# Optimization experiments

Measured on AMD Instinct MI355X. Metric: run time of the kernel, lower is better.

Reference implementation:

```python
import jax, jax.numpy as jnp
import numpy as np

ORDER = 3
OS_FACTOR = 1.5
B, T, I, H = 32, 1024, 512, 512

def _lagrange_kernel(order, os_factor):
    # mirrors LagrangeInterp_RNN.__init__
    if os_factor >= 2:
        delta = os_factor - np.floor(os_factor) + 1
    else:
        delta = os_factor - 1
    k = np.ones(order + 1, dtype=np.float64)
    for n in range(order + 1):
        for j in range(order + 1):
            if j != n:
                k[n] *= (delta - j) / (n - j)
    return jnp.asarray(k, dtype=jnp.float32)

def setup_inputs() -> dict:
    key = jax.random.key(0)
    k1, k2, k3, k4, k5 = jax.random.split(key, 5)
    s = 1.0 / np.sqrt(H)
    return {
        "x": jax.random.normal(k1, (B, T, I), dtype=jnp.float32),
        "Wih": jax.random.uniform(k2, (H, I), minval=-s, maxval=s, dtype=jnp.float32),
        "Whh": jax.random.uniform(k3, (H, H), minval=-s, maxval=s, dtype=jnp.float32),
        "bih": jax.random.uniform(k4, (H,), minval=-s, maxval=s, dtype=jnp.float32),
        "bhh": jax.random.uniform(k5, (H,), minval=-s, maxval=s, dtype=jnp.float32),
        "kernel": _lagrange_kernel(ORDER, OS_FACTOR),
    }

def reference(x, Wih, Whh, bih, bhh, kernel):
    # x: [B, T, I]; kernel: [order+1]; prev_states: [B, order+1, H]
    b = x.shape[0]
    h_dim = Whh.shape[0]
    prev0 = jnp.zeros((b, kernel.shape[0], h_dim), dtype=x.dtype)
    # input projection is independent of the recurrence -> one big GEMM
    xproj = jnp.einsum('bti,hi->bth', x, Wih) + bih  # [B, T, H]

    def step(prev, xp_t):
        # Lagrange-interpolated read of the history window
        h_read = jnp.einsum('k,bkh->bh', kernel, prev)
        h = jnp.tanh(xp_t + h_read @ Whh.T + bhh)
        # torch code detaches the state stored into prev_states, then rolls
        # so the newest (detached) state sits at index 0 (epsilon == 1)
        new_prev = jnp.concatenate(
            [jax.lax.stop_gradient(h)[:, None, :], prev[:, :-1, :]], axis=1)
        return new_prev, h

    _, states_t = jax.lax.scan(step, prev0, jnp.swapaxes(xproj, 0, 1))
    states = jnp.swapaxes(states_t, 0, 1)  # [B, T, H]
    return states, states[:, -1, :]
```

## Files before the change

kernel.cpp:

```cpp
#include <hip/hip_runtime.h>

typedef __bf16 bf16x8 __attribute__((ext_vector_type(8)));
typedef float  f32x4  __attribute__((ext_vector_type(4)));
typedef unsigned long long u64;

#define AGENT __HIP_MEMORY_SCOPE_AGENT

__device__ __forceinline__ float fast_tanh(float x) {
    float e = __expf(2.0f * x);
    return 1.0f - 2.0f * __builtin_amdgcn_rcpf(e + 1.0f);
}

__global__ __launch_bounds__(256) void xproj_gemm_kernel(
    const float* __restrict__ x, const float* __restrict__ Wih,
    const float* __restrict__ bih, float* __restrict__ out)
{
    __shared__ __bf16 Ash[64][72];
    __shared__ __bf16 Bsh[64][72];

    const int tid  = threadIdx.x;
    const int wave = tid >> 6, lane = tid & 63;
    const int col  = lane & 15, kq = lane >> 4;
    const int bt0  = blockIdx.x * 64;
    const int h0   = blockIdx.y * 64;

    f32x4 acc[4];
#pragma unroll
    for (int nt = 0; nt < 4; ++nt) acc[nt] = (f32x4){0.f, 0.f, 0.f, 0.f};

    const int r  = tid >> 2;
    const int cb = (tid & 3) * 16;

    for (int k0 = 0; k0 < 512; k0 += 64) {
        const float* ax = x   + (size_t)(bt0 + r) * 512 + k0 + cb;
        const float* bx = Wih + (size_t)(h0  + r) * 512 + k0 + cb;
#pragma unroll
        for (int j = 0; j < 4; ++j) {
            const float4 av = ((const float4*)ax)[j];
            const float4 bv = ((const float4*)bx)[j];
            const int c = cb + 4 * j;
            Ash[r][c+0]=(__bf16)av.x; Ash[r][c+1]=(__bf16)av.y;
            Ash[r][c+2]=(__bf16)av.z; Ash[r][c+3]=(__bf16)av.w;
            Bsh[r][c+0]=(__bf16)bv.x; Bsh[r][c+1]=(__bf16)bv.y;
            Bsh[r][c+2]=(__bf16)bv.z; Bsh[r][c+3]=(__bf16)bv.w;
        }
        __syncthreads();
#pragma unroll
        for (int kt = 0; kt < 2; ++kt) {
            bf16x8 a = *(const bf16x8*)&Ash[wave * 16 + col][kt * 32 + kq * 8];
#pragma unroll
            for (int nt = 0; nt < 4; ++nt) {
                bf16x8 bb = *(const bf16x8*)&Bsh[nt * 16 + col][kt * 32 + kq * 8];
                acc[nt] = __builtin_amdgcn_mfma_f32_16x16x32_bf16(a, bb, acc[nt], 0, 0, 0);
            }
        }
        __syncthreads();
    }
#pragma unroll
    for (int nt = 0; nt < 4; ++nt) {
        const float bv = bih[h0 + nt * 16 + col];
#pragma unroll
        for (int reg = 0; reg < 4; ++reg) {
            const int m = bt0 + wave * 16 + kq * 4 + reg;
            out[(size_t)m * 512 + h0 + nt * 16 + col] = acc[nt][reg] + bv;
        }
    }
}

__global__ __launch_bounds__(256) void lagrange_rnn_kernel(
    const float* __restrict__ Whh, const float* __restrict__ bhh,
    const float* __restrict__ kern, float* __restrict__ out,
    u64* __restrict__ mbox)
{
    const int id   = blockIdx.x;
    const int b    = (id & 7) + ((id >> 5) << 3);
    const int p    = (id >> 3) & 3;
    const int tid  = threadIdx.x;
    const int wave = tid >> 6, lane = tid & 63;
    const int col  = lane & 15, kq = lane >> 4;

    __shared__ float  hist[4][512];
    __shared__ __bf16 hread[2][512];

    for (int i = tid; i < 2048; i += 256) ((float*)hist)[i] = 0.f;
    for (int i = tid; i < 512;  i += 256) { hread[0][i] = (__bf16)0.f; hread[1][i] = (__bf16)0.f; }

    const int hA = p * 128 + wave * 32 + col;
    const int hB = hA + 16;
    bf16x8 wf0[16], wf1[16];
#pragma unroll
    for (int j = 0; j < 16; ++j) {
        const int ktg = ((j + 4 * p) & 15) * 32 + kq * 8;
        const float* s0 = Whh + (size_t)hA * 512 + ktg;
        const float* s1 = Whh + (size_t)hB * 512 + ktg;
        const float4 a0 = *(const float4*)s0, a1 = *(const float4*)(s0 + 4);
        const float4 b0 = *(const float4*)s1, b1 = *(const float4*)(s1 + 4);
        bf16x8 w;
        w[0]=(__bf16)a0.x; w[1]=(__bf16)a0.y; w[2]=(__bf16)a0.z; w[3]=(__bf16)a0.w;
        w[4]=(__bf16)a1.x; w[5]=(__bf16)a1.y; w[6]=(__bf16)a1.z; w[7]=(__bf16)a1.w;
        wf0[j] = w;
        w[0]=(__bf16)b0.x; w[1]=(__bf16)b0.y; w[2]=(__bf16)b0.z; w[3]=(__bf16)b0.w;
        w[4]=(__bf16)b1.x; w[5]=(__bf16)b1.y; w[6]=(__bf16)b1.z; w[7]=(__bf16)b1.w;
        wf1[j] = w;
    }
    const float k0 = kern[0], k1 = kern[1], k2 = kern[2], k3 = kern[3];
    const float bA = bhh[hA], bB = bhh[hB];
    float* stA = out + (size_t)b * 1024 * 512 + hA;
    const int peer = (p + wave) & 3;
    const int j0 = peer * 128 + lane * 2;
    const bool comp = (lane < 16);
    const int abase = p * 128 + kq * 8;

    float xA = 0.f, xB = 0.f;
    __syncthreads();
    if (comp) { xA = stA[0]; xB = stA[16]; }

    for (int t = 0; t < 1024; ++t) {
        const int rb = t & 1, wb = rb ^ 1;
        const int rt = t & 3;
        const int rm1 = (t + 3) & 3, rm2 = (t + 2) & 3, rm3 = (t + 1) & 3;
        const u64* mb_peer = mbox + (size_t)(((b << 1) | rb) * 4 + peer) * 128;

        __syncthreads();

        f32x4 acc0 = (f32x4){0,0,0,0}, acc1 = (f32x4){0,0,0,0};
#pragma unroll
        for (int j = 0; j < 4; ++j) {
            bf16x8 a = *(const bf16x8*)&hread[rb][(abase + 32 * j) & 511];
            acc0 = __builtin_amdgcn_mfma_f32_16x16x32_bf16(a, wf0[j], acc0, 0, 0, 0);
            acc1 = __builtin_amdgcn_mfma_f32_16x16x32_bf16(a, wf1[j], acc1, 0, 0, 0);
        }

        if (t && wave != 0) {
            const unsigned want = (unsigned)t;
            u64 v0, v1;
            do {
                v0 = __hip_atomic_load(&mb_peer[lane * 2],     __ATOMIC_RELAXED, AGENT);
                v1 = __hip_atomic_load(&mb_peer[lane * 2 + 1], __ATOMIC_RELAXED, AGENT);
            } while ((unsigned)(v0 >> 32) != want || (unsigned)(v1 >> 32) != want);
            union { unsigned u; float f; } d0, d1;
            d0.u = (unsigned)v0; d1.u = (unsigned)v1;
            const float q0 = k1 * hist[rm2][j0]     + k2 * hist[rm3][j0]     + k3 * hist[rt][j0];
            const float q1 = k1 * hist[rm2][j0 + 1] + k2 * hist[rm3][j0 + 1] + k3 * hist[rt][j0 + 1];
            hread[rb][j0]     = (__bf16)(q0 + k0 * d0.f);
            hread[rb][j0 + 1] = (__bf16)(q1 + k0 * d1.f);
            hist[rm1][j0]     = d0.f;
            hist[rm1][j0 + 1] = d1.f;
        }
        __syncthreads();

        float nxA = 0.f, nxB = 0.f;
        if (comp) {
            nxA = stA[(size_t)(t + 1) * 512];
            nxB = stA[(size_t)(t + 1) * 512 + 16];
        }

        float ppA = 0.f, ppB = 0.f;
        if (comp) {
            ppA = k1 * hist[rm1][hA] + k2 * hist[rm2][hA] + k3 * hist[rm3][hA];
            ppB = k1 * hist[rm1][hB] + k2 * hist[rm2][hB] + k3 * hist[rm3][hB];
        }

        f32x4 c0a = (f32x4){0,0,0,0}, c0b = (f32x4){0,0,0,0};
        f32x4 c1a = (f32x4){0,0,0,0}, c1b = (f32x4){0,0,0,0};
#pragma unroll
        for (int j = 4; j < 10; ++j) {
            bf16x8 a = *(const bf16x8*)&hread[rb][(abase + 32 * j) & 511];
            c0a = __builtin_amdgcn_mfma_f32_16x16x32_bf16(a, wf0[j], c0a, 0, 0, 0);
            c1a = __builtin_amdgcn_mfma_f32_16x16x32_bf16(a, wf1[j], c1a, 0, 0, 0);
        }
#pragma unroll
        for (int j = 10; j < 16; ++j) {
            bf16x8 a = *(const bf16x8*)&hread[rb][(abase + 32 * j) & 511];
            c0b = __builtin_amdgcn_mfma_f32_16x16x32_bf16(a, wf0[j], c0b, 0, 0, 0);
            c1b = __builtin_amdgcn_mfma_f32_16x16x32_bf16(a, wf1[j], c1b, 0, 0, 0);
        }

        if (comp) {
            const float hAv = fast_tanh(xA + acc0[0] + c0a[0] + c0b[0] + bA);
            const float hBv = fast_tanh(xB + acc1[0] + c1a[0] + c1b[0] + bB);
            u64* mb_self = mbox + (size_t)(((b << 1) | wb) * 4 + p) * 128;
            const u64 tag = (u64)(unsigned)(t + 1) << 32;
            union { float f; unsigned u; } cA, cB;
            cA.f = hAv; cB.f = hBv;
            __hip_atomic_store(&mb_self[wave * 32 + col],      tag | cA.u, __ATOMIC_RELAXED, AGENT);
            __hip_atomic_store(&mb_self[wave * 32 + col + 16], tag | cB.u, __ATOMIC_RELAXED, AGENT);
            stA[(size_t)t * 512]      = hAv;
            stA[(size_t)t * 512 + 16] = hBv;
            hist[rt][hA] = hAv;  hread[wb][hA] = (__bf16)(ppA + k0 * hAv);
            hist[rt][hB] = hBv;  hread[wb][hB] = (__bf16)(ppB + k0 * hBv);
        }
        xA = nxA; xB = nxB;
    }

    float* out2 = out + (size_t)32 * 1024 * 512 + (size_t)b * 512;
    if (comp) {
        out2[hA] = hist[3][hA];
        out2[hB] = hist[3][hB];
    }
}

extern "C" void kernel_launch(void* const* d_in, const int* in_sizes, int n_in,
                              void* d_out, int out_size, void* d_ws, size_t ws_size,
                              hipStream_t stream) {
    const float* x    = (const float*)d_in[0];
    const float* Wih  = (const float*)d_in[1];
    const float* Whh  = (const float*)d_in[2];
    const float* bih  = (const float*)d_in[3];
    const float* bhh  = (const float*)d_in[4];
    const float* kern = (const float*)d_in[5];
    float* out = (float*)d_out;

    u64* mbox = (u64*)d_ws;

    dim3 g1(512, 8, 1);
    xproj_gemm_kernel<<<g1, 256, 0, stream>>>(x, Wih, bih, out);
    lagrange_rnn_kernel<<<128, 256, 0, stream>>>(Whh, bhh, kern, out, mbox);
}
```

Measured before the change: 1.574 ms.

## Issue mailbox and xproj loads early, use LDS-only barriers, split MFMA chains

Moves the next-step xproj loads and the first mailbox poll ahead of the step's first barrier so their global latency overlaps the barrier and the early MFMAs. Replaces __syncthreads with a barrier that waits only on LDS counters, so outstanding global loads no longer stall it. Splits the remaining twelve MFMAs into three independent accumulator chains to shorten the dependency chain. The change adds register pressure, and relies on the hand-written waitcnt being enough to order the LDS traffic correctly.

```diff
diff --git a/kernel.cpp b/kernel.cpp
--- a/kernel.cpp
+++ b/kernel.cpp
@@ -9,6 +9,11 @@
 __device__ __forceinline__ float fast_tanh(float x) {
     float e = __expf(2.0f * x);
     return 1.0f - 2.0f * __builtin_amdgcn_rcpf(e + 1.0f);
+}
+
+__device__ __forceinline__ void lds_barrier() {
+    asm volatile("s_waitcnt lgkmcnt(0)" ::: "memory");
+    __builtin_amdgcn_s_barrier();
 }
 
 __global__ __launch_bounds__(256) void xproj_gemm_kernel(
@@ -120,8 +125,21 @@
         const int rt = t & 3;
         const int rm1 = (t + 3) & 3, rm2 = (t + 2) & 3, rm3 = (t + 1) & 3;
         const u64* mb_peer = mbox + (size_t)(((b << 1) | rb) * 4 + peer) * 128;
-
-        __syncthreads();
+        const bool polling = (t != 0) && (wave != 0);
+        const unsigned want = (unsigned)t;
+
+        float nxA = 0.f, nxB = 0.f;
+        if (comp) {
+            nxA = stA[(size_t)(t + 1) * 512];
+            nxB = stA[(size_t)(t + 1) * 512 + 16];
+        }
+        u64 v0 = 0, v1 = 0;
+        if (polling) {
+            v0 = __hip_atomic_load(&mb_peer[lane * 2],     __ATOMIC_RELAXED, AGENT);
+            v1 = __hip_atomic_load(&mb_peer[lane * 2 + 1], __ATOMIC_RELAXED, AGENT);
+        }
+
+        lds_barrier();
 
         f32x4 acc0 = (f32x4){0,0,0,0}, acc1 = (f32x4){0,0,0,0};
 #pragma unroll
@@ -131,13 +149,11 @@
             acc1 = __builtin_amdgcn_mfma_f32_16x16x32_bf16(a, wf1[j], acc1, 0, 0, 0);
         }
 
-        if (t && wave != 0) {
-            const unsigned want = (unsigned)t;
-            u64 v0, v1;
-            do {
+        if (polling) {
+            while ((unsigned)(v0 >> 32) != want || (unsigned)(v1 >> 32) != want) {
                 v0 = __hip_atomic_load(&mb_peer[lane * 2],     __ATOMIC_RELAXED, AGENT);
                 v1 = __hip_atomic_load(&mb_peer[lane * 2 + 1], __ATOMIC_RELAXED, AGENT);
-            } while ((unsigned)(v0 >> 32) != want || (unsigned)(v1 >> 32) != want);
+            }
             union { unsigned u; float f; } d0, d1;
             d0.u = (unsigned)v0; d1.u = (unsigned)v1;
             const float q0 = k1 * hist[rm2][j0]     + k2 * hist[rm3][j0]     + k3 * hist[rt][j0];
@@ -147,13 +163,8 @@
             hist[rm1][j0]     = d0.f;
             hist[rm1][j0 + 1] = d1.f;
         }
-        __syncthreads();
-
-        float nxA = 0.f, nxB = 0.f;
-        if (comp) {
-            nxA = stA[(size_t)(t + 1) * 512];
-            nxB = stA[(size_t)(t + 1) * 512 + 16];
-        }
+
+        lds_barrier();
 
         float ppA = 0.f, ppB = 0.f;
         if (comp) {
@@ -161,24 +172,30 @@
             ppB = k1 * hist[rm1][hB] + k2 * hist[rm2][hB] + k3 * hist[rm3][hB];
         }
 
-        f32x4 c0a = (f32x4){0,0,0,0}, c0b = (f32x4){0,0,0,0};
-        f32x4 c1a = (f32x4){0,0,0,0}, c1b = (f32x4){0,0,0,0};
-#pragma unroll
-        for (int j = 4; j < 10; ++j) {
+        f32x4 c0a = (f32x4){0,0,0,0}, c0b = (f32x4){0,0,0,0}, c0c = (f32x4){0,0,0,0};
+        f32x4 c1a = (f32x4){0,0,0,0}, c1b = (f32x4){0,0,0,0}, c1c = (f32x4){0,0,0,0};
+#pragma unroll
+        for (int j = 4; j < 8; ++j) {
             bf16x8 a = *(const bf16x8*)&hread[rb][(abase + 32 * j) & 511];
             c0a = __builtin_amdgcn_mfma_f32_16x16x32_bf16(a, wf0[j], c0a, 0, 0, 0);
             c1a = __builtin_amdgcn_mfma_f32_16x16x32_bf16(a, wf1[j], c1a, 0, 0, 0);
         }
 #pragma unroll
-        for (int j = 10; j < 16; ++j) {
+        for (int j = 8; j < 12; ++j) {
             bf16x8 a = *(const bf16x8*)&hread[rb][(abase + 32 * j) & 511];
             c0b = __builtin_amdgcn_mfma_f32_16x16x32_bf16(a, wf0[j], c0b, 0, 0, 0);
             c1b = __builtin_amdgcn_mfma_f32_16x16x32_bf16(a, wf1[j], c1b, 0, 0, 0);
         }
+#pragma unroll
+        for (int j = 12; j < 16; ++j) {
+            bf16x8 a = *(const bf16x8*)&hread[rb][(abase + 32 * j) & 511];
+            c0c = __builtin_amdgcn_mfma_f32_16x16x32_bf16(a, wf0[j], c0c, 0, 0, 0);
+            c1c = __builtin_amdgcn_mfma_f32_16x16x32_bf16(a, wf1[j], c1c, 0, 0, 0);
+        }
 
         if (comp) {
-            const float hAv = fast_tanh(xA + acc0[0] + c0a[0] + c0b[0] + bA);
-            const float hBv = fast_tanh(xB + acc1[0] + c1a[0] + c1b[0] + bB);
+            const float hAv = fast_tanh(xA + acc0[0] + c0a[0] + c0b[0] + c0c[0] + bA);
+            const float hBv = fast_tanh(xB + acc1[0] + c1a[0] + c1b[0] + c1c[0] + bB);
             u64* mb_self = mbox + (size_t)(((b << 1) | wb) * 4 + p) * 128;
             const u64 tag = (u64)(unsigned)(t + 1) << 32;
             union { float f; unsigned u; } cA, cB;
```

Result: faster. 1.301 ms (-17.3%).
